# Kernel tuning notes

Hardware: AMD Instinct MI355X
Metric: run time of the kernel (lower is better)

Reference implementation:

```python
import jax, jax.numpy as jnp
import numpy as np

LAMBDA_PROTO = 0.5
EPS = 1e-12  # F.normalize eps


def setup_inputs() -> dict:
    key = jax.random.key(0)
    k1, k2, k3 = jax.random.split(key, 3)
    N, D, C = 262144, 128, 64
    emb = jax.random.normal(k1, (N, D), dtype=jnp.float32)
    logits = jax.random.normal(k2, (N, C), dtype=jnp.float32)
    labels = jax.random.randint(k3, (N,), 0, C, dtype=jnp.int64)
    return {"emb": emb, "logits": logits, "labels": labels}


def reference(emb, logits, labels):
    N, D = emb.shape
    C = logits.shape[1]

    # F.normalize(emb, dim=1): x / max(||x||, eps)
    nrm = jnp.sqrt(jnp.sum(emb * emb, axis=1, keepdims=True))
    z = emb / jnp.maximum(nrm, EPS)

    # Cross-entropy (mean reduction, no class weights)
    logp = jax.nn.log_softmax(logits, axis=-1)
    ce = -jnp.mean(jnp.take_along_axis(logp, labels[:, None], axis=1))

    # Per-class stats via segment reduce (single fused pass, no python loop)
    lab = labels.astype(jnp.int32)
    counts = jax.ops.segment_sum(jnp.ones((N,), jnp.float32), lab, num_segments=C)  # [C]
    sums = jax.ops.segment_sum(z, lab, num_segments=C)                               # [C, D]
    sq = jax.ops.segment_sum(jnp.sum(z * z, axis=1), lab, num_segments=C)            # [C]

    safe_n = jnp.maximum(counts, 1.0)
    mu = sums / safe_n[:, None]
    # sum_i ||z_i - mu||^2 = sum_i ||z_i||^2 - n * ||mu||^2
    ssd = sq - counts * jnp.sum(mu * mu, axis=1)
    per_class = ssd / safe_n  # mean over samples of squared distance

    valid = counts > 1.0  # classes with <=1 sample are skipped
    n_valid = jnp.sum(valid.astype(jnp.float32))
    proto_loss = jnp.sum(jnp.where(valid, per_class, 0.0)) / jnp.maximum(n_valid, 1.0)

    return (1.0 - LAMBDA_PROTO) * ce + LAMBDA_PROTO * proto_loss
```

## Files before the change

### kernel.cpp

```cpp
#include <hip/hip_runtime.h>
#include <math.h>

#define N_ROWS 262144
#define D 128
#define C 64
#define NB1 2048
#define RPB1 128
#define SCB 512
#define CSTRIDE 4608
#define PB 1024
#define PT 512
#define TMAX 9
#define OCTW 132

#define OFF_HIST   0
#define OFF_BASES  (NB1 * C)
#define OFF_IDX    (2 * NB1 * C)
#define OFF_CNT    (2 * NB1 * C + C * CSTRIDE)
#define OFF_CEB    (OFF_CNT + C)
#define OFF_OCT    (OFF_CEB + NB1)
#define OFF_RES    (OFF_OCT + PB * OCTW)

__global__ __launch_bounds__(256, 8) void ce_hist_kernel(
    const float* __restrict__ logits, const int* __restrict__ labels,
    float* __restrict__ ceB, int* __restrict__ hist) {
  __shared__ float sCe[4];
  __shared__ int sH[C];
  const int tid = threadIdx.x;
  if (tid < C) sH[tid] = 0;
  __syncthreads();

  const int wave = tid >> 6, lane = tid & 63;
  const int g = lane >> 4, lp = lane & 15;
  const int rowBase = blockIdx.x * RPB1 + wave * 32 + g;
  float ce_acc = 0.f;

  float4 tA, tB;
  int labA = 0, labB = 0;
  tA = *(const float4*)(logits + (size_t)rowBase * C + lp * 4);
  labA = labels[rowBase];
  tB = tA;

#pragma unroll
  for (int it = 0; it < 8; ++it) {
    const float4 t4 = (it & 1) ? tB : tA;
    const int lab = (it & 1) ? labB : labA;
    if (it + 1 < 8) {
      const int row = rowBase + (it + 1) * 4;
      if (it & 1) {
        tA = *(const float4*)(logits + (size_t)row * C + lp * 4);
        labA = labels[row];
      } else {
        tB = *(const float4*)(logits + (size_t)row * C + lp * 4);
        labB = labels[row];
      }
    }
    float p = __expf(t4.x) + __expf(t4.y) + __expf(t4.z) + __expf(t4.w);
    float tl = 0.f;
    if ((lab >> 2) == lp) {
      const int k = lab & 3;
      tl = k == 0 ? t4.x : k == 1 ? t4.y : k == 2 ? t4.z : t4.w;
    }
    p += __shfl_xor(p, 1);  tl += __shfl_xor(tl, 1);
    p += __shfl_xor(p, 2);  tl += __shfl_xor(tl, 2);
    p += __shfl_xor(p, 4);  tl += __shfl_xor(tl, 4);
    p += __shfl_xor(p, 8);  tl += __shfl_xor(tl, 8);
    if (lp == 0) {
      ce_acc += __logf(p) - tl;
      atomicAdd(&sH[lab], 1);
    }
  }
  ce_acc += __shfl_xor(ce_acc, 16);
  ce_acc += __shfl_xor(ce_acc, 32);
  if (lane == 0) sCe[wave] = ce_acc;
  __syncthreads();
  if (tid == 0) ceB[blockIdx.x] = sCe[0] + sCe[1] + sCe[2] + sCe[3];
  if (tid < C) hist[blockIdx.x * C + tid] = sH[tid];
}

__global__ __launch_bounds__(256) void scan_kernel(
    const int* __restrict__ hist, int* __restrict__ bases,
    int* __restrict__ cnts) {
  __shared__ int sA[256], sB[256];
  const int c = blockIdx.x, t = threadIdx.x;
  int h[8], tot = 0;
#pragma unroll
  for (int j = 0; j < 8; ++j) {
    h[j] = hist[(t * 8 + j) * C + c];
    tot += h[j];
  }
  sA[t] = tot;
  __syncthreads();
#pragma unroll
  for (int st = 0; st < 8; ++st) {
    const int off = 1 << st;
    if (st & 1) sA[t] = sB[t] + ((t >= off) ? sB[t - off] : 0);
    else        sB[t] = sA[t] + ((t >= off) ? sA[t - off] : 0);
    __syncthreads();
  }
  const int incl = sA[t];
  int run = incl - tot;
#pragma unroll
  for (int j = 0; j < 8; ++j) {
    bases[(t * 8 + j) * C + c] = run;
    run += h[j];
  }
  if (t == 255) cnts[c] = incl;
}

__global__ __launch_bounds__(512) void scatter_kernel(
    const int* __restrict__ labels, const int* __restrict__ bases,
    int* __restrict__ idx) {
  __shared__ int sCur[C];
  const int t = threadIdx.x, b = blockIdx.x;
  if (t < C) sCur[t] = bases[(b * 4) * C + t];
  __syncthreads();
  const int row = b * 512 + t;
  const int lab = labels[row];
  const int pos = atomicAdd(&sCur[lab], 1);
  idx[lab * CSTRIDE + pos] = row;
}

__global__ __launch_bounds__(PT, 4) void proto_kernel(
    const float* __restrict__ emb, const int* __restrict__ idxArr,
    const int* __restrict__ cnts, float* __restrict__ oct) {
  const int tid = threadIdx.x;
  const int wave = tid >> 6, lane = tid & 63;
  const int g = lane >> 4, lp = lane & 15;
  const int c = blockIdx.x >> 4, o = blockIdx.x & 15;
  const int gg = o * 32 + wave * 4 + g;
  const int n = cnts[c];
  const int nm1 = (n > 0) ? n - 1 : 0;
  const int* ip = idxArr + c * CSTRIDE;

  int rI[TMAX];
#pragma unroll
  for (int t = 0; t < TMAX; ++t) {
    const int e = gg + 512 * t;
    rI[t] = ip[e < nm1 ? e : nm1];
  }

  float4 s0a, s0b, s1a, s1b, s2a, s2b, s3a, s3b, s4a, s4b, s5a, s5b;
  {
    const float* p0 = emb + (size_t)rI[0] * D + lp * 8;
    s0a = *(const float4*)p0;  s0b = *(const float4*)(p0 + 4);
    const float* p1 = emb + (size_t)rI[1] * D + lp * 8;
    s1a = *(const float4*)p1;  s1b = *(const float4*)(p1 + 4);
    const float* p2 = emb + (size_t)rI[2] * D + lp * 8;
    s2a = *(const float4*)p2;  s2b = *(const float4*)(p2 + 4);
    const float* p3 = emb + (size_t)rI[3] * D + lp * 8;
    s3a = *(const float4*)p3;  s3b = *(const float4*)(p3 + 4);
    const float* p4 = emb + (size_t)rI[4] * D + lp * 8;
    s4a = *(const float4*)p4;  s4b = *(const float4*)(p4 + 4);
    const float* p5 = emb + (size_t)rI[5] * D + lp * 8;
    s5a = *(const float4*)p5;  s5b = *(const float4*)(p5 + 4);
  }

  float4 accA = {0.f, 0.f, 0.f, 0.f}, accB = {0.f, 0.f, 0.f, 0.f};
  float cnt = 0.f, sq = 0.f;

#pragma unroll
  for (int t = 0; t < TMAX; ++t) {
    const int r6 = t % 6;
    const float4 ea = r6 == 0 ? s0a : r6 == 1 ? s1a : r6 == 2 ? s2a
                    : r6 == 3 ? s3a : r6 == 4 ? s4a : s5a;
    const float4 eb = r6 == 0 ? s0b : r6 == 1 ? s1b : r6 == 2 ? s2b
                    : r6 == 3 ? s3b : r6 == 4 ? s4b : s5b;
    if (t + 6 < TMAX) {
      const float* pn = emb + (size_t)rI[t + 6] * D + lp * 8;
      if (r6 == 0)      { s0a = *(const float4*)pn; s0b = *(const float4*)(pn + 4); }
      else if (r6 == 1) { s1a = *(const float4*)pn; s1b = *(const float4*)(pn + 4); }
      else              { s2a = *(const float4*)pn; s2b = *(const float4*)(pn + 4); }
    }
    float ss = ea.x * ea.x + ea.y * ea.y + ea.z * ea.z + ea.w * ea.w +
               eb.x * eb.x + eb.y * eb.y + eb.z * eb.z + eb.w * eb.w;
    ss += __shfl_xor(ss, 1);
    ss += __shfl_xor(ss, 2);
    ss += __shfl_xor(ss, 4);
    ss += __shfl_xor(ss, 8);
    const float inv = 1.0f / fmaxf(sqrtf(ss), 1e-12f);
    const bool valid = (gg + 512 * t) < n;
    const float sc = valid ? inv : 0.f;
    accA.x += ea.x * sc;  accA.y += ea.y * sc;
    accA.z += ea.z * sc;  accA.w += ea.w * sc;
    accB.x += eb.x * sc;  accB.y += eb.y * sc;
    accB.z += eb.z * sc;  accB.w += eb.w * sc;
    if (lp == 0) {
      cnt += valid ? 1.f : 0.f;
      sq += valid ? ss * inv * inv : 0.f;
    }
  }

#pragma unroll
  for (int off = 16; off <= 32; off <<= 1) {
    accA.x += __shfl_xor(accA.x, off);  accA.y += __shfl_xor(accA.y, off);
    accA.z += __shfl_xor(accA.z, off);  accA.w += __shfl_xor(accA.w, off);
    accB.x += __shfl_xor(accB.x, off);  accB.y += __shfl_xor(accB.y, off);
    accB.z += __shfl_xor(accB.z, off);  accB.w += __shfl_xor(accB.w, off);
    cnt += __shfl_xor(cnt, off);
    sq += __shfl_xor(sq, off);
  }

  __shared__ float sR[8][OCTW];
  if (lane < 16) {
    *(float4*)&sR[wave][lp * 8] = accA;
    *(float4*)&sR[wave][lp * 8 + 4] = accB;
  }
  if (lane == 0) { sR[wave][128] = cnt; sR[wave][129] = sq; }
  __syncthreads();
  if (tid < 130) {
    float s = 0.f;
#pragma unroll
    for (int w = 0; w < 8; ++w) s += sR[w][tid];
    oct[(size_t)blockIdx.x * OCTW + tid] = s;
  }
}

__global__ __launch_bounds__(128) void class_kernel(
    const float* __restrict__ oct, float* __restrict__ res) {
  __shared__ float sM[2];
  const int c = blockIdx.x, t = threadIdx.x;
  float s = 0.f, n = 0.f, sq = 0.f;
#pragma unroll
  for (int o = 0; o < 16; ++o) {
    const float* f = oct + (size_t)(c * 16 + o) * OCTW;
    s += f[t];
    n += f[128];
    sq += f[129];
  }
  const float safe = fmaxf(n, 1.f);
  const float mu = s / safe;
  float msq = mu * mu;
#pragma unroll
  for (int off = 1; off < 64; off <<= 1) msq += __shfl_xor(msq, off);
  if ((t & 63) == 0) sM[t >> 6] = msq;
  __syncthreads();
  if (t == 0) {
    const float ssd = sq - n * (sM[0] + sM[1]);
    const bool valid = n > 1.f;
    res[c] = valid ? ssd / safe : 0.f;
    res[C + c] = valid ? 1.f : 0.f;
  }
}

__global__ __launch_bounds__(256) void final_kernel(
    const float* __restrict__ ceB, const float* __restrict__ res,
    float* __restrict__ out) {
  __shared__ float sv[4][3];
  const int tid = threadIdx.x, wave = tid >> 6, lane = tid & 63;
  float ce = 0.f;
  for (int i = tid; i < NB1; i += 256) ce += ceB[i];
  float pr = 0.f, nv = 0.f;
  if (wave == 0) { pr = res[lane]; nv = res[C + lane]; }
#pragma unroll
  for (int off = 1; off < 64; off <<= 1) {
    ce += __shfl_xor(ce, off);
    pr += __shfl_xor(pr, off);
    nv += __shfl_xor(nv, off);
  }
  if (lane == 0) { sv[wave][0] = ce; sv[wave][1] = pr; sv[wave][2] = nv; }
  __syncthreads();
  if (tid == 0) {
    const float c2 = sv[0][0] + sv[1][0] + sv[2][0] + sv[3][0];
    const float p2 = sv[0][1] + sv[1][1] + sv[2][1] + sv[3][1];
    const float n2 = sv[0][2] + sv[1][2] + sv[2][2] + sv[3][2];
    out[0] = 0.5f * (c2 / (float)N_ROWS) + 0.5f * (p2 / fmaxf(n2, 1.f));
  }
}

extern "C" void kernel_launch(void* const* d_in, const int* in_sizes, int n_in,
                              void* d_out, int out_size, void* d_ws, size_t ws_size,
                              hipStream_t stream) {
  const float* emb = (const float*)d_in[0];
  const float* logits = (const float*)d_in[1];
  const int* labels = (const int*)d_in[2];
  int* wsi = (int*)d_ws;
  float* wsf = (float*)d_ws;
  float* out = (float*)d_out;

  int* hist = wsi + OFF_HIST;
  int* bases = wsi + OFF_BASES;
  int* idx = wsi + OFF_IDX;
  int* cnts = wsi + OFF_CNT;
  float* ceB = wsf + OFF_CEB;
  float* oct = wsf + OFF_OCT;
  float* res = wsf + OFF_RES;

  ce_hist_kernel<<<NB1, 256, 0, stream>>>(logits, labels, ceB, hist);
  scan_kernel<<<C, 256, 0, stream>>>(hist, bases, cnts);
  scatter_kernel<<<SCB, 512, 0, stream>>>(labels, bases, idx);
  proto_kernel<<<PB, PT, 0, stream>>>(emb, idx, cnts, oct);
  class_kernel<<<C, 128, 0, stream>>>(oct, res);
  final_kernel<<<1, 256, 0, stream>>>(ceB, res, out);
}
```

Baseline: 54.63 us.

## Fuse cross-entropy into proto kernel and shrink histogram pass to labels only

Moves the cross-entropy computation out of the first histogram kernel and into the prototype kernel. Odd and even blocks run the CE and proto phases in opposite order so that logits streaming overlaps the gathered embedding loads. The histogram kernel now reads only labels with 512 blocks, so the scan and scatter kernels change their indexing to match. This shortens the serial chain before the proto work, at the cost of more register pressure and a longer fused kernel.

```diff
diff --git a/kernel.cpp b/kernel.cpp
--- a/kernel.cpp
+++ b/kernel.cpp
@@ -4,77 +4,31 @@
 #define N_ROWS 262144
 #define D 128
 #define C 64
-#define NB1 2048
-#define RPB1 128
-#define SCB 512
+#define HB 512
 #define CSTRIDE 4608
-#define PB 1024
-#define PT 512
+#define FB 1024
+#define FT 512
 #define TMAX 9
 #define OCTW 132
 
 #define OFF_HIST   0
-#define OFF_BASES  (NB1 * C)
-#define OFF_IDX    (2 * NB1 * C)
-#define OFF_CNT    (2 * NB1 * C + C * CSTRIDE)
+#define OFF_BASES  (HB * C)
+#define OFF_IDX    (2 * HB * C)
+#define OFF_CNT    (2 * HB * C + C * CSTRIDE)
 #define OFF_CEB    (OFF_CNT + C)
-#define OFF_OCT    (OFF_CEB + NB1)
-#define OFF_RES    (OFF_OCT + PB * OCTW)
-
-__global__ __launch_bounds__(256, 8) void ce_hist_kernel(
-    const float* __restrict__ logits, const int* __restrict__ labels,
-    float* __restrict__ ceB, int* __restrict__ hist) {
-  __shared__ float sCe[4];
+#define OFF_OCT    (OFF_CEB + FB)
+#define OFF_RES    (OFF_OCT + FB * OCTW)
+
+__global__ __launch_bounds__(256) void hist_kernel(
+    const int* __restrict__ labels, int* __restrict__ hist) {
   __shared__ int sH[C];
   const int tid = threadIdx.x;
   if (tid < C) sH[tid] = 0;
   __syncthreads();
-
-  const int wave = tid >> 6, lane = tid & 63;
-  const int g = lane >> 4, lp = lane & 15;
-  const int rowBase = blockIdx.x * RPB1 + wave * 32 + g;
-  float ce_acc = 0.f;
-
-  float4 tA, tB;
-  int labA = 0, labB = 0;
-  tA = *(const float4*)(logits + (size_t)rowBase * C + lp * 4);
-  labA = labels[rowBase];
-  tB = tA;
-
-#pragma unroll
-  for (int it = 0; it < 8; ++it) {
-    const float4 t4 = (it & 1) ? tB : tA;
-    const int lab = (it & 1) ? labB : labA;
-    if (it + 1 < 8) {
-      const int row = rowBase + (it + 1) * 4;
-      if (it & 1) {
-        tA = *(const float4*)(logits + (size_t)row * C + lp * 4);
-        labA = labels[row];
-      } else {
-        tB = *(const float4*)(logits + (size_t)row * C + lp * 4);
-        labB = labels[row];
-      }
-    }
-    float p = __expf(t4.x) + __expf(t4.y) + __expf(t4.z) + __expf(t4.w);
-    float tl = 0.f;
-    if ((lab >> 2) == lp) {
-      const int k = lab & 3;
-      tl = k == 0 ? t4.x : k == 1 ? t4.y : k == 2 ? t4.z : t4.w;
-    }
-    p += __shfl_xor(p, 1);  tl += __shfl_xor(tl, 1);
-    p += __shfl_xor(p, 2);  tl += __shfl_xor(tl, 2);
-    p += __shfl_xor(p, 4);  tl += __shfl_xor(tl, 4);
-    p += __shfl_xor(p, 8);  tl += __shfl_xor(tl, 8);
-    if (lp == 0) {
-      ce_acc += __logf(p) - tl;
-      atomicAdd(&sH[lab], 1);
-    }
-  }
-  ce_acc += __shfl_xor(ce_acc, 16);
-  ce_acc += __shfl_xor(ce_acc, 32);
-  if (lane == 0) sCe[wave] = ce_acc;
-  __syncthreads();
-  if (tid == 0) ceB[blockIdx.x] = sCe[0] + sCe[1] + sCe[2] + sCe[3];
+  const int2 l = *(const int2*)(labels + blockIdx.x * 512 + tid * 2);
+  atomicAdd(&sH[l.x], 1);
+  atomicAdd(&sH[l.y], 1);
+  __syncthreads();
   if (tid < C) hist[blockIdx.x * C + tid] = sH[tid];
 }
 
@@ -83,12 +37,9 @@
     int* __restrict__ cnts) {
   __shared__ int sA[256], sB[256];
   const int c = blockIdx.x, t = threadIdx.x;
-  int h[8], tot = 0;
-#pragma unroll
-  for (int j = 0; j < 8; ++j) {
-    h[j] = hist[(t * 8 + j) * C + c];
-    tot += h[j];
-  }
+  const int h0 = hist[(2 * t) * C + c];
+  const int h1 = hist[(2 * t + 1) * C + c];
+  const int tot = h0 + h1;
   sA[t] = tot;
   __syncthreads();
 #pragma unroll
@@ -99,12 +50,9 @@
     __syncthreads();
   }
   const int incl = sA[t];
-  int run = incl - tot;
-#pragma unroll
-  for (int j = 0; j < 8; ++j) {
-    bases[(t * 8 + j) * C + c] = run;
-    run += h[j];
-  }
+  const int excl = incl - tot;
+  bases[(2 * t) * C + c] = excl;
+  bases[(2 * t + 1) * C + c] = excl + h0;
   if (t == 255) cnts[c] = incl;
 }
 
@@ -113,7 +61,7 @@
     int* __restrict__ idx) {
   __shared__ int sCur[C];
   const int t = threadIdx.x, b = blockIdx.x;
-  if (t < C) sCur[t] = bases[(b * 4) * C + t];
+  if (t < C) sCur[t] = bases[b * C + t];
   __syncthreads();
   const int row = b * 512 + t;
   const int lab = labels[row];
@@ -121,99 +69,156 @@
   idx[lab * CSTRIDE + pos] = row;
 }
 
-__global__ __launch_bounds__(PT, 4) void proto_kernel(
-    const float* __restrict__ emb, const int* __restrict__ idxArr,
-    const int* __restrict__ cnts, float* __restrict__ oct) {
+__global__ __launch_bounds__(FT, 4) void fused_kernel(
+    const float* __restrict__ emb, const float* __restrict__ logits,
+    const int* __restrict__ labels, const int* __restrict__ idxArr,
+    const int* __restrict__ cnts, float* __restrict__ ceB,
+    float* __restrict__ oct) {
+  __shared__ float sCe[8];
+  __shared__ float sR[8][OCTW];
+
   const int tid = threadIdx.x;
   const int wave = tid >> 6, lane = tid & 63;
   const int g = lane >> 4, lp = lane & 15;
-  const int c = blockIdx.x >> 4, o = blockIdx.x & 15;
-  const int gg = o * 32 + wave * 4 + g;
-  const int n = cnts[c];
-  const int nm1 = (n > 0) ? n - 1 : 0;
-  const int* ip = idxArr + c * CSTRIDE;
-
-  int rI[TMAX];
-#pragma unroll
-  for (int t = 0; t < TMAX; ++t) {
-    const int e = gg + 512 * t;
-    rI[t] = ip[e < nm1 ? e : nm1];
-  }
-
-  float4 s0a, s0b, s1a, s1b, s2a, s2b, s3a, s3b, s4a, s4b, s5a, s5b;
-  {
-    const float* p0 = emb + (size_t)rI[0] * D + lp * 8;
-    s0a = *(const float4*)p0;  s0b = *(const float4*)(p0 + 4);
-    const float* p1 = emb + (size_t)rI[1] * D + lp * 8;
-    s1a = *(const float4*)p1;  s1b = *(const float4*)(p1 + 4);
-    const float* p2 = emb + (size_t)rI[2] * D + lp * 8;
-    s2a = *(const float4*)p2;  s2b = *(const float4*)(p2 + 4);
-    const float* p3 = emb + (size_t)rI[3] * D + lp * 8;
-    s3a = *(const float4*)p3;  s3b = *(const float4*)(p3 + 4);
-    const float* p4 = emb + (size_t)rI[4] * D + lp * 8;
-    s4a = *(const float4*)p4;  s4b = *(const float4*)(p4 + 4);
-    const float* p5 = emb + (size_t)rI[5] * D + lp * 8;
-    s5a = *(const float4*)p5;  s5b = *(const float4*)(p5 + 4);
-  }
-
-  float4 accA = {0.f, 0.f, 0.f, 0.f}, accB = {0.f, 0.f, 0.f, 0.f};
-  float cnt = 0.f, sq = 0.f;
-
-#pragma unroll
-  for (int t = 0; t < TMAX; ++t) {
-    const int r6 = t % 6;
-    const float4 ea = r6 == 0 ? s0a : r6 == 1 ? s1a : r6 == 2 ? s2a
-                    : r6 == 3 ? s3a : r6 == 4 ? s4a : s5a;
-    const float4 eb = r6 == 0 ? s0b : r6 == 1 ? s1b : r6 == 2 ? s2b
-                    : r6 == 3 ? s3b : r6 == 4 ? s4b : s5b;
-    if (t + 6 < TMAX) {
-      const float* pn = emb + (size_t)rI[t + 6] * D + lp * 8;
-      if (r6 == 0)      { s0a = *(const float4*)pn; s0b = *(const float4*)(pn + 4); }
-      else if (r6 == 1) { s1a = *(const float4*)pn; s1b = *(const float4*)(pn + 4); }
-      else              { s2a = *(const float4*)pn; s2b = *(const float4*)(pn + 4); }
-    }
-    float ss = ea.x * ea.x + ea.y * ea.y + ea.z * ea.z + ea.w * ea.w +
-               eb.x * eb.x + eb.y * eb.y + eb.z * eb.z + eb.w * eb.w;
-    ss += __shfl_xor(ss, 1);
-    ss += __shfl_xor(ss, 2);
-    ss += __shfl_xor(ss, 4);
-    ss += __shfl_xor(ss, 8);
-    const float inv = 1.0f / fmaxf(sqrtf(ss), 1e-12f);
-    const bool valid = (gg + 512 * t) < n;
-    const float sc = valid ? inv : 0.f;
-    accA.x += ea.x * sc;  accA.y += ea.y * sc;
-    accA.z += ea.z * sc;  accA.w += ea.w * sc;
-    accB.x += eb.x * sc;  accB.y += eb.y * sc;
-    accB.z += eb.z * sc;  accB.w += eb.w * sc;
-    if (lp == 0) {
-      cnt += valid ? 1.f : 0.f;
-      sq += valid ? ss * inv * inv : 0.f;
-    }
-  }
-
-#pragma unroll
-  for (int off = 16; off <= 32; off <<= 1) {
-    accA.x += __shfl_xor(accA.x, off);  accA.y += __shfl_xor(accA.y, off);
-    accA.z += __shfl_xor(accA.z, off);  accA.w += __shfl_xor(accA.w, off);
-    accB.x += __shfl_xor(accB.x, off);  accB.y += __shfl_xor(accB.y, off);
-    accB.z += __shfl_xor(accB.z, off);  accB.w += __shfl_xor(accB.w, off);
-    cnt += __shfl_xor(cnt, off);
-    sq += __shfl_xor(sq, off);
-  }
-
-  __shared__ float sR[8][OCTW];
-  if (lane < 16) {
-    *(float4*)&sR[wave][lp * 8] = accA;
-    *(float4*)&sR[wave][lp * 8 + 4] = accB;
-  }
-  if (lane == 0) { sR[wave][128] = cnt; sR[wave][129] = sq; }
-  __syncthreads();
-  if (tid < 130) {
-    float s = 0.f;
-#pragma unroll
-    for (int w = 0; w < 8; ++w) s += sR[w][tid];
-    oct[(size_t)blockIdx.x * OCTW + tid] = s;
-  }
+  const int b = blockIdx.x;
+
+  auto ce_phase = [&]() {
+    const int rowBase = b * 256 + wave * 32 + g;
+    float ce_acc = 0.f;
+    float4 tA, tB;
+    int labA = 0, labB = 0;
+    tA = *(const float4*)(logits + (size_t)rowBase * C + lp * 4);
+    labA = labels[rowBase];
+    tB = tA;
+#pragma unroll
+    for (int it = 0; it < 8; ++it) {
+      const float4 t4 = (it & 1) ? tB : tA;
+      const int lab = (it & 1) ? labB : labA;
+      if (it + 1 < 8) {
+        const int row = rowBase + (it + 1) * 4;
+        if (it & 1) {
+          tA = *(const float4*)(logits + (size_t)row * C + lp * 4);
+          labA = labels[row];
+        } else {
+          tB = *(const float4*)(logits + (size_t)row * C + lp * 4);
+          labB = labels[row];
+        }
+      }
+      float p = __expf(t4.x) + __expf(t4.y) + __expf(t4.z) + __expf(t4.w);
+      float tl = 0.f;
+      if ((lab >> 2) == lp) {
+        const int k = lab & 3;
+        tl = k == 0 ? t4.x : k == 1 ? t4.y : k == 2 ? t4.z : t4.w;
+      }
+      p += __shfl_xor(p, 1);  tl += __shfl_xor(tl, 1);
+      p += __shfl_xor(p, 2);  tl += __shfl_xor(tl, 2);
+      p += __shfl_xor(p, 4);  tl += __shfl_xor(tl, 4);
+      p += __shfl_xor(p, 8);  tl += __shfl_xor(tl, 8);
+      if (lp == 0) ce_acc += __logf(p) - tl;
+    }
+    ce_acc += __shfl_xor(ce_acc, 16);
+    ce_acc += __shfl_xor(ce_acc, 32);
+    if (lane == 0) sCe[wave] = ce_acc;
+    __syncthreads();
+    if (tid == 0) {
+      float s = 0.f;
+#pragma unroll
+      for (int w = 0; w < 8; ++w) s += sCe[w];
+      ceB[b] = s;
+    }
+  };
+
+  auto proto_phase = [&]() {
+    const int c = b >> 4, o = b & 15;
+    const int gg = o * 32 + wave * 4 + g;
+    const int n = cnts[c];
+    const int nm1 = (n > 0) ? n - 1 : 0;
+    const int* ip = idxArr + c * CSTRIDE;
+
+    int rI[TMAX];
+#pragma unroll
+    for (int t = 0; t < TMAX; ++t) {
+      const int e = gg + 512 * t;
+      rI[t] = ip[e < nm1 ? e : nm1];
+    }
+
+    float4 s0a, s0b, s1a, s1b, s2a, s2b, s3a, s3b, s4a, s4b, s5a, s5b;
+    {
+      const float* p0 = emb + (size_t)rI[0] * D + lp * 8;
+      s0a = *(const float4*)p0;  s0b = *(const float4*)(p0 + 4);
+      const float* p1 = emb + (size_t)rI[1] * D + lp * 8;
+      s1a = *(const float4*)p1;  s1b = *(const float4*)(p1 + 4);
+      const float* p2 = emb + (size_t)rI[2] * D + lp * 8;
+      s2a = *(const float4*)p2;  s2b = *(const float4*)(p2 + 4);
+      const float* p3 = emb + (size_t)rI[3] * D + lp * 8;
+      s3a = *(const float4*)p3;  s3b = *(const float4*)(p3 + 4);
+      const float* p4 = emb + (size_t)rI[4] * D + lp * 8;
+      s4a = *(const float4*)p4;  s4b = *(const float4*)(p4 + 4);
+      const float* p5 = emb + (size_t)rI[5] * D + lp * 8;
+      s5a = *(const float4*)p5;  s5b = *(const float4*)(p5 + 4);
+    }
+
+    float4 accA = {0.f, 0.f, 0.f, 0.f}, accB = {0.f, 0.f, 0.f, 0.f};
+    float cnt = 0.f, sq = 0.f;
+
+#pragma unroll
+    for (int t = 0; t < TMAX; ++t) {
+      const int r6 = t % 6;
+      const float4 ea = r6 == 0 ? s0a : r6 == 1 ? s1a : r6 == 2 ? s2a
+                      : r6 == 3 ? s3a : r6 == 4 ? s4a : s5a;
+      const float4 eb = r6 == 0 ? s0b : r6 == 1 ? s1b : r6 == 2 ? s2b
+                      : r6 == 3 ? s3b : r6 == 4 ? s4b : s5b;
+      if (t + 6 < TMAX) {
+        const float* pn = emb + (size_t)rI[t + 6] * D + lp * 8;
+        if (r6 == 0)      { s0a = *(const float4*)pn; s0b = *(const float4*)(pn + 4); }
+        else if (r6 == 1) { s1a = *(const float4*)pn; s1b = *(const float4*)(pn + 4); }
+        else              { s2a = *(const float4*)pn; s2b = *(const float4*)(pn + 4); }
+      }
+      float ss = ea.x * ea.x + ea.y * ea.y + ea.z * ea.z + ea.w * ea.w +
+                 eb.x * eb.x + eb.y * eb.y + eb.z * eb.z + eb.w * eb.w;
+      ss += __shfl_xor(ss, 1);
+      ss += __shfl_xor(ss, 2);
+      ss += __shfl_xor(ss, 4);
+      ss += __shfl_xor(ss, 8);
+      const float inv = 1.0f / fmaxf(sqrtf(ss), 1e-12f);
+      const bool valid = (gg + 512 * t) < n;
+      const float sc = valid ? inv : 0.f;
+      accA.x += ea.x * sc;  accA.y += ea.y * sc;
+      accA.z += ea.z * sc;  accA.w += ea.w * sc;
+      accB.x += eb.x * sc;  accB.y += eb.y * sc;
+      accB.z += eb.z * sc;  accB.w += eb.w * sc;
+      if (lp == 0) {
+        cnt += valid ? 1.f : 0.f;
+        sq += valid ? ss * inv * inv : 0.f;
+      }
+    }
+
+#pragma unroll
+    for (int off = 16; off <= 32; off <<= 1) {
+      accA.x += __shfl_xor(accA.x, off);  accA.y += __shfl_xor(accA.y, off);
+      accA.z += __shfl_xor(accA.z, off);  accA.w += __shfl_xor(accA.w, off);
+      accB.x += __shfl_xor(accB.x, off);  accB.y += __shfl_xor(accB.y, off);
+      accB.z += __shfl_xor(accB.z, off);  accB.w += __shfl_xor(accB.w, off);
+      cnt += __shfl_xor(cnt, off);
+      sq += __shfl_xor(sq, off);
+    }
+
+    if (lane < 16) {
+      *(float4*)&sR[wave][lp * 8] = accA;
+      *(float4*)&sR[wave][lp * 8 + 4] = accB;
+    }
+    if (lane == 0) { sR[wave][128] = cnt; sR[wave][129] = sq; }
+    __syncthreads();
+    if (tid < 130) {
+      float s = 0.f;
+#pragma unroll
+      for (int w = 0; w < 8; ++w) s += sR[w][tid];
+      oct[(size_t)b * OCTW + tid] = s;
+    }
+  };
+
+  if (b & 1) { ce_phase(); __syncthreads(); proto_phase(); }
+  else       { proto_phase(); __syncthreads(); ce_phase(); }
 }
 
 __global__ __launch_bounds__(128) void class_kernel(
@@ -249,7 +254,7 @@
   __shared__ float sv[4][3];
   const int tid = threadIdx.x, wave = tid >> 6, lane = tid & 63;
   float ce = 0.f;
-  for (int i = tid; i < NB1; i += 256) ce += ceB[i];
+  for (int i = tid; i < FB; i += 256) ce += ceB[i];
   float pr = 0.f, nv = 0.f;
   if (wave == 0) { pr = res[lane]; nv = res[C + lane]; }
 #pragma unroll
@@ -286,10 +291,10 @@
   float* oct = wsf + OFF_OCT;
   float* res = wsf + OFF_RES;
 
-  ce_hist_kernel<<<NB1, 256, 0, stream>>>(logits, labels, ceB, hist);
+  hist_kernel<<<HB, 256, 0, stream>>>(labels, hist);
   scan_kernel<<<C, 256, 0, stream>>>(hist, bases, cnts);
-  scatter_kernel<<<SCB, 512, 0, stream>>>(labels, bases, idx);
-  proto_kernel<<<PB, PT, 0, stream>>>(emb, idx, cnts, oct);
+  scatter_kernel<<<HB, 512, 0, stream>>>(labels, bases, idx);
+  fused_kernel<<<FB, FT, 0, stream>>>(emb, logits, labels, idx, cnts, ceB, oct);
   class_kernel<<<C, 128, 0, stream>>>(oct, res);
   final_kernel<<<1, 256, 0, stream>>>(ceB, res, out);
 }
```

Measured after the change: 54.57 us. About the same (-0.1%).
